# Performance work log

Hardware: AMD Instinct MI355X
Metric: run time of the kernel (lower is better)

The kernel has to match this reference:

```python
import jax, jax.numpy as jnp
import numpy as np

POOL = 7
IMAGE_SHAPE = (1024, 1024, 3)


def _crop_and_resize(fmap, boxes, pool):
    """TF-style crop_and_resize with extrapolation_value=0.
    fmap: [C, H, W]; boxes: [N, (y1,x1,y2,x2)] normalized. Returns [N, C, pool, pool]."""
    C, H, W = fmap.shape
    dt = fmap.dtype
    y1, x1, y2, x2 = boxes[:, 0], boxes[:, 1], boxes[:, 2], boxes[:, 3]
    g = jnp.arange(pool, dtype=dt) / (pool - 1)  # [P] in [0,1]
    ys = (y1[:, None] + g[None, :] * (y2 - y1)[:, None]) * (H - 1)  # [N,P]
    xs = (x1[:, None] + g[None, :] * (x2 - x1)[:, None]) * (W - 1)  # [N,P]
    y0f = jnp.floor(ys); x0f = jnp.floor(xs)
    ly = (ys - y0f).astype(dt); lx = (xs - x0f).astype(dt)
    y0 = jnp.clip(y0f.astype(jnp.int32), 0, H - 1)
    y1i = jnp.clip(y0 + 1, 0, H - 1)
    x0 = jnp.clip(x0f.astype(jnp.int32), 0, W - 1)
    x1i = jnp.clip(x0 + 1, 0, W - 1)
    vy = ((ys >= 0) & (ys <= H - 1)).astype(dt)  # extrapolation_value = 0 outside
    vx = ((xs >= 0) & (xs <= W - 1)).astype(dt)

    def at(yi, xi):
        # gather -> [C, N, P, P]
        return fmap[:, yi[:, :, None], xi[:, None, :]]

    wy0 = (1 - ly)[None, :, :, None]; wy1 = ly[None, :, :, None]
    wx0 = (1 - lx)[None, :, None, :]; wx1 = lx[None, :, None, :]
    val = (at(y0, x0) * wy0 + at(y1i, x0) * wy1) * wx0 \
        + (at(y0, x1i) * wy0 + at(y1i, x1i) * wy1) * wx1
    val = val * (vy[None, :, :, None] * vx[None, :, None, :])
    return jnp.transpose(val, (1, 0, 2, 3))  # [N, C, P, P]


def reference(boxes, p2, p3, p4, p5):
    """pyramid_roi_align: route each box to FPN level 2..5 via the 224-scale
    log2 heuristic, then CropAndResize(pool, pool, 0) from that level.
    Output order matches input box order (original sorts back by box_to_level)."""
    h = boxes[:, 2] - boxes[:, 0]
    w = boxes[:, 3] - boxes[:, 1]
    image_area = float(IMAGE_SHAPE[0] * IMAGE_SHAPE[1])
    roi_level = 4.0 + jnp.log2(jnp.sqrt(h * w) / (224.0 / np.sqrt(image_area)))
    roi_level = jnp.clip(jnp.round(roi_level).astype(jnp.int32), 2, 5)
    boxes_d = jax.lax.stop_gradient(boxes)  # level_boxes.detach() in original
    fmaps = [p2, p3, p4, p5]
    pooled = jnp.zeros((boxes.shape[0], p2.shape[0], POOL, POOL), dtype=p2.dtype)
    for i, level in enumerate(range(2, 6)):
        mask = (roi_level == level).astype(p2.dtype)[:, None, None, None]
        pooled = pooled + mask * _crop_and_resize(fmaps[i], boxes_d, POOL)
    return pooled


def setup_inputs():
    key = jax.random.key(0)
    kb, ks, k2, k3, k4, k5 = jax.random.split(key, 6)
    N, C = 1000, 256
    size = jax.random.uniform(ks, (N, 2), minval=0.02, maxval=0.9)
    tl = jax.random.uniform(kb, (N, 2)) * (1.0 - size)  # top-left so box stays in [0,1]
    boxes = jnp.concatenate([tl[:, 0:1], tl[:, 1:2],
                             tl[:, 0:1] + size[:, 0:1], tl[:, 1:2] + size[:, 1:2]], axis=1)
    p2 = jax.random.normal(k2, (C, 256, 256), jnp.float32)
    p3 = jax.random.normal(k3, (C, 128, 128), jnp.float32)
    p4 = jax.random.normal(k4, (C, 64, 64), jnp.float32)
    p5 = jax.random.normal(k5, (C, 32, 32), jnp.float32)
    return {"boxes": boxes, "p2": p2, "p3": p3, "p4": p4, "p5": p5}
```

## Files before the change

### kernel.cpp

```cpp
#include <hip/hip_runtime.h>


#define POOL 7
#define NCH  256
#define ELEMS_PER_BOX (NCH * POOL * POOL)
#define HALF_ELEMS (ELEMS_PER_BOX / 2)
#define CG 8
#define NGROUPS 16
#define ROWS 14
#define SA 32
#define SROW 36
#define GROUP_OUT (CG * 49)

typedef float f2 __attribute__((ext_vector_type(2)));
typedef float f4 __attribute__((ext_vector_type(4)));

__global__ __launch_bounds__(256, 8) void roi_align_kernel(
    const float* __restrict__ boxes,
    const float* __restrict__ p2, const float* __restrict__ p3,
    const float* __restrict__ p4, const float* __restrict__ p5,
    float* __restrict__ out, int N)
{
    const int bid  = blockIdx.x;
    const int n    = bid >> 1;
    const int half = bid & 1;

    __shared__ float s_stage[CG * ROWS * SROW];
    __shared__ float s_a[49], s_b[49], s_w0[49], s_w1[49];
    __shared__ int   s_dx[49];
    __shared__ int   s_off0[49], s_off1[49];
    __shared__ int   s_rowoff[ROWS];
    __shared__ int   s_HW, s_xb0a, s_sa4, s_fast;
    __shared__ const float* s_fmap;

    const int tid = threadIdx.x;

    if (tid < 49) {
        const float by1 = boxes[4 * n + 0];
        const float bx1 = boxes[4 * n + 1];
        const float by2 = boxes[4 * n + 2];
        const float bx2 = boxes[4 * n + 3];
        const float h = by2 - by1;
        const float w = bx2 - bx1;
        float rl = 4.0f + log2f(sqrtf(h * w) / 0.21875f);
        int level = (int)rintf(rl);
        level = min(5, max(2, level));
        const int H = 256 >> (level - 2);
        const int W = H;
        const int py = tid / 7;
        const int px = tid - 7 * py;

        const float ty = (float)py / 6.0f;
        const float ys = (by1 + ty * (by2 - by1)) * (float)(H - 1);
        const float yf = floorf(ys);
        const float ly = ys - yf;
        int y0 = (int)yf; y0 = min(H - 1, max(0, y0));
        const int y1 = min(H - 1, y0 + 1);
        const float vy = (ys >= 0.0f && ys <= (float)(H - 1)) ? 1.0f : 0.0f;

        const float tx = (float)px / 6.0f;
        const float xs = (bx1 + tx * (bx2 - bx1)) * (float)(W - 1);
        const float xf = floorf(xs);
        const float lx = xs - xf;
        int x0 = (int)xf; x0 = min(W - 1, max(0, x0));
        const float vx = (xs >= 0.0f && xs <= (float)(W - 1)) ? 1.0f : 0.0f;
        const int xb = min(x0, W - 2);
        const bool edge = (x0 != xb);
        const float a = edge ? 0.0f : vx * (1.0f - lx);
        const float b = edge ? vx : vx * lx;

        const float xsA = (bx1 + 0.0f * (bx2 - bx1)) * (float)(W - 1);
        int xA = (int)floorf(xsA); xA = min(W - 1, max(0, xA));
        const int xbA = min(xA, W - 2);
        const float xsB = (bx1 + 1.0f * (bx2 - bx1)) * (float)(W - 1);
        int xB = (int)floorf(xsB); xB = min(W - 1, max(0, xB));
        const int xbB = min(xB, W - 2);
        const int xb0a = min(xbA & ~3, W - SA);
        const int need = xbB + 2 - xb0a;

        s_off0[tid] = y0 * W + xb;
        s_off1[tid] = y1 * W + xb;
        s_a[tid] = a;
        s_b[tid] = b;
        s_w0[tid] = vy * (1.0f - ly);
        s_w1[tid] = vy * ly;
        s_dx[tid] = xb - xb0a;
        if (px == 0) {
            s_rowoff[2 * py]     = y0 * W;
            s_rowoff[2 * py + 1] = y1 * W;
        }
        if (tid == 0) {
            s_HW = H * W;
            s_fmap = (level == 2) ? p2 : (level == 3) ? p3 : (level == 4) ? p4 : p5;
            s_xb0a = xb0a;
            s_sa4  = (need + 3) >> 2;
            s_fast = (need <= SA) ? 1 : 0;
        }
    }
    __syncthreads();

    const int HW = s_HW;
    const float* __restrict__ fbase = s_fmap + (size_t)(half * 128) * HW;
    float* __restrict__ op = out + (size_t)n * ELEMS_PER_BOX + half * HALF_ELEMS;

    const int c1  = tid / 49,  p1  = tid - 49 * c1;
    const int o2  = 256 + tid;
    const int c2  = o2 / 49,   p2i = o2 - 49 * c2;
    const bool act2 = (tid < GROUP_OUT - 256);

    const float a1 = s_a[p1],  b1 = s_b[p1],  w01 = s_w0[p1],  w11 = s_w1[p1];
    const float a2 = s_a[p2i], b2 = s_b[p2i], w02 = s_w0[p2i], w12 = s_w1[p2i];

    if (s_fast) {
        const int sa4  = s_sa4;
        const int xb0a = s_xb0a;

        int goff[4], lw[4];
        bool gact[4];
#pragma unroll
        for (int pp = 0; pp < 4; ++pp) {
            const int idx = pp * 256 + tid;
            const int rid = idx >> 3;
            const int q   = idx & 7;
            gact[pp] = (rid < CG * ROWS) && (q < sa4);
            const int cl = rid / 14;
            const int r  = rid - 14 * cl;
            lw[pp]   = rid * SROW + q * 4;
            goff[pp] = cl * HW + s_rowoff[r] + xb0a + q * 4;
        }

        const int t1 = (c1 * ROWS + 2 * (p1 / 7)) * SROW + s_dx[p1];
        const int t2 = (c2 * ROWS + 2 * (p2i / 7)) * SROW + s_dx[p2i];

        for (int g = 0; g < NGROUPS; ++g) {
            const float* fg = fbase + (size_t)(g * CG) * HW;
            f4 v[4];
#pragma unroll
            for (int pp = 0; pp < 4; ++pp)
                if (gact[pp]) v[pp] = *(const f4*)(fg + goff[pp]);
#pragma unroll
            for (int pp = 0; pp < 4; ++pp)
                if (gact[pp]) *(f4*)(&s_stage[lw[pp]]) = v[pp];
            __syncthreads();

            {
                const float t00 = s_stage[t1],        t01 = s_stage[t1 + 1];
                const float t10 = s_stage[t1 + SROW], t11 = s_stage[t1 + SROW + 1];
                const float r0 = t00 * a1 + t01 * b1;
                const float r1 = t10 * a1 + t11 * b1;
                op[g * GROUP_OUT + tid] = r0 * w01 + r1 * w11;
            }
            if (act2) {
                const float u00 = s_stage[t2],        u01 = s_stage[t2 + 1];
                const float u10 = s_stage[t2 + SROW], u11 = s_stage[t2 + SROW + 1];
                const float s0 = u00 * a2 + u01 * b2;
                const float s1 = u10 * a2 + u11 * b2;
                op[g * GROUP_OUT + 256 + tid] = s0 * w02 + s1 * w12;
            }
            __syncthreads();
        }
    } else {
        const int off01 = s_off0[p1],  off11 = s_off1[p1];
        const int off02 = s_off0[p2i], off12 = s_off1[p2i];
        for (int g = 0; g < NGROUPS; ++g) {
            const float* pl1 = fbase + (size_t)(g * CG + c1) * HW;
            const f2 q0 = *(const f2*)(pl1 + off01);
            const f2 q1 = *(const f2*)(pl1 + off11);
            const float r0 = q0.x * a1 + q0.y * b1;
            const float r1 = q1.x * a1 + q1.y * b1;
            op[g * GROUP_OUT + tid] = r0 * w01 + r1 * w11;
            if (act2) {
                const float* pl2 = fbase + (size_t)(g * CG + c2) * HW;
                const f2 u0 = *(const f2*)(pl2 + off02);
                const f2 u1 = *(const f2*)(pl2 + off12);
                const float s0 = u0.x * a2 + u0.y * b2;
                const float s1 = u1.x * a2 + u1.y * b2;
                op[g * GROUP_OUT + 256 + tid] = s0 * w02 + s1 * w12;
            }
        }
    }
}

extern "C" void kernel_launch(void* const* d_in, const int* in_sizes, int n_in,
                              void* d_out, int out_size, void* d_ws, size_t ws_size,
                              hipStream_t stream) {
    const float* boxes = (const float*)d_in[0];
    const float* p2    = (const float*)d_in[1];
    const float* p3    = (const float*)d_in[2];
    const float* p4    = (const float*)d_in[3];
    const float* p5    = (const float*)d_in[4];
    float* out = (float*)d_out;
    const int N = in_sizes[0] / 4;

    roi_align_kernel<<<N * 2, 256, 0, stream>>>(boxes, p2, p3, p4, p5, out, N);
}
```

Baseline: 169.2 us.

## Double-buffer LDS staging with register prefetch and split boxes into channel quarters

Each box is now split across four blocks of 64 channels instead of two blocks of 128, which doubles the grid and lowers the launch-bounds occupancy hint from 8 to 4. The fast path becomes a two-buffer LDS pipeline: the global loads for the next channel group are issued into registers while the current group is interpolated, with one barrier per stage. The aim is to hide global-load latency and raise parallelism in a latency-bound gather. The costs are more register pressure, twice the LDS staging space, and the per-box setup being repeated across four blocks. The fast-path window now starts at the aligned box start without clamping to W-SA, and eligibility is tested on the rounded quad count.

```diff
diff --git a/kernel.cpp b/kernel.cpp
--- a/kernel.cpp
+++ b/kernel.cpp
@@ -4,33 +4,35 @@
 #define POOL 7
 #define NCH  256
 #define ELEMS_PER_BOX (NCH * POOL * POOL)
-#define HALF_ELEMS (ELEMS_PER_BOX / 2)
+#define QCH 64
+#define QELEMS (QCH * POOL * POOL)
 #define CG 8
-#define NGROUPS 16
+#define NGROUPS (QCH / CG)
 #define ROWS 14
 #define SA 32
 #define SROW 36
+#define BUFSZ (CG * ROWS * SROW)
 #define GROUP_OUT (CG * 49)
 
 typedef float f2 __attribute__((ext_vector_type(2)));
 typedef float f4 __attribute__((ext_vector_type(4)));
 
-__global__ __launch_bounds__(256, 8) void roi_align_kernel(
+__global__ __launch_bounds__(256, 4) void roi_align_kernel(
     const float* __restrict__ boxes,
     const float* __restrict__ p2, const float* __restrict__ p3,
     const float* __restrict__ p4, const float* __restrict__ p5,
     float* __restrict__ out, int N)
 {
     const int bid  = blockIdx.x;
-    const int n    = bid >> 1;
-    const int half = bid & 1;
-
-    __shared__ float s_stage[CG * ROWS * SROW];
+    const int n    = bid >> 2;
+    const int quarter = bid & 3;
+
+    __shared__ float s_stage[2][BUFSZ];
     __shared__ float s_a[49], s_b[49], s_w0[49], s_w1[49];
     __shared__ int   s_dx[49];
     __shared__ int   s_off0[49], s_off1[49];
     __shared__ int   s_rowoff[ROWS];
-    __shared__ int   s_HW, s_xb0a, s_sa4, s_fast;
+    __shared__ int   s_HW, s_xb0, s_sa4, s_fast;
     __shared__ const float* s_fmap;
 
     const int tid = threadIdx.x;
@@ -69,14 +71,14 @@
         const float a = edge ? 0.0f : vx * (1.0f - lx);
         const float b = edge ? vx : vx * lx;
 
-        const float xsA = (bx1 + 0.0f * (bx2 - bx1)) * (float)(W - 1);
+        const float xsA = bx1 * (float)(W - 1);
         int xA = (int)floorf(xsA); xA = min(W - 1, max(0, xA));
         const int xbA = min(xA, W - 2);
-        const float xsB = (bx1 + 1.0f * (bx2 - bx1)) * (float)(W - 1);
+        const float xsB = bx2 * (float)(W - 1);
         int xB = (int)floorf(xsB); xB = min(W - 1, max(0, xB));
         const int xbB = min(xB, W - 2);
-        const int xb0a = min(xbA & ~3, W - SA);
-        const int need = xbB + 2 - xb0a;
+        const int xb0 = xbA & ~3;
+        const int sa4 = ((xbB + 2 - xb0) + 3) >> 2;
 
         s_off0[tid] = y0 * W + xb;
         s_off1[tid] = y1 * W + xb;
@@ -84,7 +86,7 @@
         s_b[tid] = b;
         s_w0[tid] = vy * (1.0f - ly);
         s_w1[tid] = vy * ly;
-        s_dx[tid] = xb - xb0a;
+        s_dx[tid] = xb - xb0;
         if (px == 0) {
             s_rowoff[2 * py]     = y0 * W;
             s_rowoff[2 * py + 1] = y1 * W;
@@ -92,16 +94,16 @@
         if (tid == 0) {
             s_HW = H * W;
             s_fmap = (level == 2) ? p2 : (level == 3) ? p3 : (level == 4) ? p4 : p5;
-            s_xb0a = xb0a;
-            s_sa4  = (need + 3) >> 2;
-            s_fast = (need <= SA) ? 1 : 0;
+            s_xb0 = xb0;
+            s_sa4 = sa4;
+            s_fast = (sa4 <= (SA / 4)) ? 1 : 0;
         }
     }
     __syncthreads();
 
     const int HW = s_HW;
-    const float* __restrict__ fbase = s_fmap + (size_t)(half * 128) * HW;
-    float* __restrict__ op = out + (size_t)n * ELEMS_PER_BOX + half * HALF_ELEMS;
+    const float* __restrict__ fbase = s_fmap + (size_t)(quarter * QCH) * HW;
+    float* __restrict__ op = out + (size_t)n * ELEMS_PER_BOX + quarter * QELEMS;
 
     const int c1  = tid / 49,  p1  = tid - 49 * c1;
     const int o2  = 256 + tid;
@@ -112,8 +114,8 @@
     const float a2 = s_a[p2i], b2 = s_b[p2i], w02 = s_w0[p2i], w12 = s_w1[p2i];
 
     if (s_fast) {
-        const int sa4  = s_sa4;
-        const int xb0a = s_xb0a;
+        const int sa4 = s_sa4;
+        const int xb0 = s_xb0;
 
         int goff[4], lw[4];
         bool gact[4];
@@ -126,39 +128,57 @@
             const int cl = rid / 14;
             const int r  = rid - 14 * cl;
             lw[pp]   = rid * SROW + q * 4;
-            goff[pp] = cl * HW + s_rowoff[r] + xb0a + q * 4;
+            goff[pp] = cl * HW + s_rowoff[r] + xb0 + q * 4;
         }
 
         const int t1 = (c1 * ROWS + 2 * (p1 / 7)) * SROW + s_dx[p1];
         const int t2 = (c2 * ROWS + 2 * (p2i / 7)) * SROW + s_dx[p2i];
 
-        for (int g = 0; g < NGROUPS; ++g) {
-            const float* fg = fbase + (size_t)(g * CG) * HW;
-            f4 v[4];
+        f4 va[4], vb[4];
+
+#define STAGE(vv, g)                                                          \
+        {                                                                     \
+            const float* fg = fbase + (size_t)((g) * CG) * HW;                \
+            _Pragma("unroll")                                                 \
+            for (int pp = 0; pp < 4; ++pp)                                    \
+                if (gact[pp]) vv[pp] = *(const f4*)(fg + goff[pp]);           \
+        }
+#define LDSWRITE(buf, vv)                                                     \
+        {                                                                     \
+            _Pragma("unroll")                                                 \
+            for (int pp = 0; pp < 4; ++pp)                                    \
+                if (gact[pp]) *(f4*)(&s_stage[buf][lw[pp]]) = vv[pp];         \
+        }
+#define COMPUTE(g, buf)                                                       \
+        {                                                                     \
+            const float* st = s_stage[buf];                                   \
+            const float t00 = st[t1],        t01 = st[t1 + 1];                \
+            const float t10 = st[t1 + SROW], t11 = st[t1 + SROW + 1];         \
+            op[(g) * GROUP_OUT + tid] =                                       \
+                (t00 * a1 + t01 * b1) * w01 + (t10 * a1 + t11 * b1) * w11;    \
+            if (act2) {                                                       \
+                const float u00 = st[t2],        u01 = st[t2 + 1];            \
+                const float u10 = st[t2 + SROW], u11 = st[t2 + SROW + 1];     \
+                op[(g) * GROUP_OUT + 256 + tid] =                             \
+                    (u00 * a2 + u01 * b2) * w02 + (u10 * a2 + u11 * b2) * w12;\
+            }                                                                 \
+        }
+
+        STAGE(va, 0);
 #pragma unroll
-            for (int pp = 0; pp < 4; ++pp)
-                if (gact[pp]) v[pp] = *(const f4*)(fg + goff[pp]);
-#pragma unroll
-            for (int pp = 0; pp < 4; ++pp)
-                if (gact[pp]) *(f4*)(&s_stage[lw[pp]]) = v[pp];
+        for (int g = 0; g < NGROUPS; g += 2) {
+            LDSWRITE(0, va);
+            STAGE(vb, g + 1);
             __syncthreads();
-
-            {
-                const float t00 = s_stage[t1],        t01 = s_stage[t1 + 1];
-                const float t10 = s_stage[t1 + SROW], t11 = s_stage[t1 + SROW + 1];
-                const float r0 = t00 * a1 + t01 * b1;
-                const float r1 = t10 * a1 + t11 * b1;
-                op[g * GROUP_OUT + tid] = r0 * w01 + r1 * w11;
-            }
-            if (act2) {
-                const float u00 = s_stage[t2],        u01 = s_stage[t2 + 1];
-                const float u10 = s_stage[t2 + SROW], u11 = s_stage[t2 + SROW + 1];
-                const float s0 = u00 * a2 + u01 * b2;
-                const float s1 = u10 * a2 + u11 * b2;
-                op[g * GROUP_OUT + 256 + tid] = s0 * w02 + s1 * w12;
-            }
+            COMPUTE(g, 0);
+            LDSWRITE(1, vb);
+            if (g + 2 < NGROUPS) STAGE(va, g + 2);
             __syncthreads();
-        }
+            COMPUTE(g + 1, 1);
+        }
+#undef STAGE
+#undef LDSWRITE
+#undef COMPUTE
     } else {
         const int off01 = s_off0[p1],  off11 = s_off1[p1];
         const int off02 = s_off0[p2i], off12 = s_off1[p2i];
@@ -192,5 +212,5 @@
     float* out = (float*)d_out;
     const int N = in_sizes[0] / 4;
 
-    roi_align_kernel<<<N * 2, 256, 0, stream>>>(boxes, p2, p3, p4, p5, out, N);
+    roi_align_kernel<<<N * 4, 256, 0, stream>>>(boxes, p2, p3, p4, p5, out, N);
 }
```

New measurement: 214.2 us. 1.27x slower.
